# Kernel optimization log

Hardware: AMD Instinct MI355X
Metric: run time of the kernel (lower is better)

Reference implementation:

```python
import jax, jax.numpy as jnp
import numpy as np

NUM_HEADS = 8
HIDDEN = 256


def _coattention(qf, rf, Wq, bq, Wk, bk, Wv, bv, Wo, bo, rel_emb):
    # qf, rf: (b, c, h, w); attention is axial over the height axis per width column.
    b, c, h, w = qf.shape
    T = rel_emb.shape[0]  # 2*max(h,w)-1
    q_in = qf.reshape(b, c, h * w).transpose(0, 2, 1)  # b (hw) c
    r_in = rf.reshape(b, c, h * w).transpose(0, 2, 1)
    q = (q_in @ Wq + bq).reshape(b, h, w, NUM_HEADS, HIDDEN).transpose(0, 3, 1, 2, 4)  # b n h w c
    k = (r_in @ Wk + bk).reshape(b, h, w, NUM_HEADS, HIDDEN).transpose(0, 3, 1, 2, 4)
    v = (r_in @ Wv + bv).reshape(b, h, w, NUM_HEADS, HIDDEN).transpose(0, 3, 1, 2, 4)
    scores = jnp.einsum('bnhwc,bnkwc->bnhwk', q, k)
    # relative index table: idx[i, j] = j - i, wrapped like torch negative indexing
    idx_h = (jnp.arange(h)[None, :] - jnp.arange(h)[:, None]) % T  # (h, h)
    idx_w = (jnp.arange(w)[None, :] - jnp.arange(w)[:, None]) % T  # (w, w); h == w required
    rel_h = rel_emb[idx_h]  # (h, h, c)
    rel_w = rel_emb[idx_w]  # (w, w, c)
    scores = scores + jnp.einsum('bnhwc,hkc->bnhwk', q, rel_h)
    scores = scores + jnp.einsum('bnhwc,wkc->bnhwk', q, rel_w)
    probs = jax.nn.softmax(scores / np.float32(np.sqrt(HIDDEN)), axis=-1)
    att = jnp.einsum('bnhwk,bnkwc->bnhwc', probs, v)
    out = att.transpose(0, 2, 3, 1, 4).reshape(b, h * w, NUM_HEADS * HIDDEN)  # b (hw) (n c)
    out = out @ Wo + bo
    return out.transpose(0, 2, 1).reshape(b, c, h, w)


def setup_inputs() -> dict:
    key = jax.random.key(0)
    ks = jax.random.split(key, 8)
    B, C, H, W = 4, 2048, 32, 32
    s = np.float32(0.02)
    return {
        'left_features': jax.random.normal(ks[0], (B, C, H, W), jnp.float32),
        'right_features': jax.random.normal(ks[1], (B, C, H, W), jnp.float32),
        'Wq': jax.random.normal(ks[2], (C, C), jnp.float32) * s,
        'bq': jnp.zeros((C,), jnp.float32),
        'Wk': jax.random.normal(ks[3], (C, C), jnp.float32) * s,
        'bk': jnp.zeros((C,), jnp.float32),
        'Wv': jax.random.normal(ks[4], (C, C), jnp.float32) * s,
        'bv': jnp.zeros((C,), jnp.float32),
        'Wo': jax.random.normal(ks[5], (C, C), jnp.float32) * s,
        'bo': jnp.zeros((C,), jnp.float32),
        'rel_emb': jax.random.normal(ks[6], (2 * max(H, W) - 1, HIDDEN), jnp.float32),
    }


def reference(left_features, right_features, Wq, bq, Wk, bk, Wv, bv, Wo, bo, rel_emb):
    weighted_r = _coattention(left_features, right_features, Wq, bq, Wk, bk, Wv, bv, Wo, bo, rel_emb)
    weighted_l = _coattention(right_features, left_features, Wq, bq, Wk, bk, Wv, bv, Wo, bo, rel_emb)
    left_attended = jnp.concatenate([left_features, weighted_r], axis=1)
    right_attended = jnp.concatenate([right_features, weighted_l], axis=1)
    return (left_attended, right_attended)
```

## Files before the change

### kernel.cpp

```cpp
#include <hip/hip_runtime.h>
#include <hip/hip_bf16.h>

typedef __attribute__((ext_vector_type(8))) short bf16x8;
typedef __attribute__((ext_vector_type(4))) float f32x4;

#define MFMA16(a, b, c) __builtin_amdgcn_mfma_f32_16x16x32_bf16((a), (b), (c), 0, 0, 0)

typedef __attribute__((address_space(1))) const void gconst_t;
typedef __attribute__((address_space(3))) void lds_t;
__device__ __forceinline__ void gload16(const void* gp, void* lp) {
    __builtin_amdgcn_global_load_lds((gconst_t*)gp, (lds_t*)lp, 16, 0, 0);
}

#define BAR() asm volatile("s_barrier" ::: "memory")
#define VMCNT0() asm volatile("s_waitcnt vmcnt(0)" ::: "memory")
#define DRAIN() asm volatile("s_waitcnt vmcnt(0) lgkmcnt(0)" ::: "memory")
#define PRIO1() __builtin_amdgcn_s_setprio(1)
#define PRIO0() __builtin_amdgcn_s_setprio(0)
#define SCHED0() __builtin_amdgcn_sched_barrier(0)

struct PArgs {
    const float* w[4];
    __hip_bfloat16* wt[4];
    const float* x[2];
    __hip_bfloat16* xb[2];
    const float* rel;
    __hip_bfloat16* relb;
    float* out;
};
__global__ void prep(PArgs pa) {
    __shared__ float tile[32][33];
    const int z = blockIdx.z;
    const int tx = threadIdx.x, ty = threadIdx.y;
    if (z < 4) {
        const float* __restrict__ ib = pa.w[z];
        __hip_bfloat16* __restrict__ ob = pa.wt[z];
        int r0 = blockIdx.y * 32, c0 = blockIdx.x * 32;
#pragma unroll
        for (int i = ty; i < 32; i += 8)
            tile[i][tx] = ib[(size_t)(r0 + i) * 2048 + c0 + tx];
        __syncthreads();
#pragma unroll
        for (int i = ty; i < 32; i += 8)
            ob[(size_t)(c0 + i) * 2048 + r0 + tx] = __float2bfloat16(tile[tx][i]);
    } else {
        const int zb = z - 4;
        const int side = blockIdx.x >> 5;
        size_t zoff = (size_t)zb * 2048 * 1024;
        const float* __restrict__ ib = pa.x[side] + zoff;
        __hip_bfloat16* __restrict__ ob = pa.xb[side] + zoff;
        float* __restrict__ cb = pa.out + (size_t)side * 16777216 + (size_t)zb * 4194304;
        int r0 = blockIdx.y * 32, c0 = (blockIdx.x & 31) * 32;
#pragma unroll
        for (int i = ty; i < 32; i += 8) {
            float v = ib[(size_t)(r0 + i) * 1024 + c0 + tx];
            tile[i][tx] = v;
            cb[(size_t)(r0 + i) * 1024 + c0 + tx] = v;
        }
        __syncthreads();
#pragma unroll
        for (int i = ty; i < 32; i += 8)
            ob[(size_t)(c0 + i) * 2048 + r0 + tx] = __float2bfloat16(tile[tx][i]);
        if (z == 4 && blockIdx.x == 0 && blockIdx.y == 0) {
            int tid = ty * 32 + tx;
            for (int i = tid; i < 64 * 256; i += 256) {
                int r = i >> 8;
                pa.relb[i] = __float2bfloat16(r < 63 ? pa.rel[i] : 0.f);
            }
        }
    }
}

struct GArgs {
    const __hip_bfloat16* A[6];
    const __hip_bfloat16* B[6];
    void* C[6];
    const float* bias[6];
};

template <int MODE>
__global__ __launch_bounds__(512, 2) void gemm8p(GArgs ga, float* __restrict__ dout) {
    constexpr int K = 2048;
    constexpr int NOUT = 2048;
    constexpr int NT = 32;
    __shared__ __align__(16) char smem[131072];

    const int gx = gridDim.x, gy = gridDim.y;
    int lid = blockIdx.x + gx * (blockIdx.y + gy * blockIdx.z);
    const int nwg = gx * gy * gridDim.z;
    int swz = (lid & 7) * (nwg >> 3) + (lid >> 3);
    const int z = swz / (gx * gy);
    int rem = swz - z * (gx * gy);
    const int by = rem / gx;
    const int bx = rem - by * gx;

    const __hip_bfloat16* __restrict__ A = ga.A[z];
    const __hip_bfloat16* __restrict__ B = ga.B[z];
    const float* __restrict__ bias = ga.bias[z];
    const int row0 = by * 256, col0 = bx * 256;

    const int tid = threadIdx.x;
    const int wave = tid >> 6, lane = tid & 63;
    const int l15 = lane & 15, lg = lane >> 4;
    const int wm = wave >> 2, wn = wave & 3;

    const int srow = tid >> 3;
    const int sch = (tid & 7) ^ (srow & 7);
    const int xr = (l15 & 7) << 4;
    const int off0 = (lg * 16) ^ xr;
    const int off1 = (64 + lg * 16) ^ xr;

    f32x4 acc[8][4] = {};
    bf16x8 aL[4][2], aH[4][2], bL[2][2], bH[2][2];

    auto ST = [&](const __hip_bfloat16* base, int rowb, int T, int buf, int isB, int h) {
#pragma unroll
        for (int L = 0; L < 2; ++L)
            gload16(base + (size_t)(rowb + h * 128 + L * 64 + srow) * K + T * 64 + sch * 8,
                    smem + buf * 65536 + isB * 32768 + h * 16384 + L * 8192 + tid * 16);
    };

#define RD_A(DST, C, MH)                                                           \
    _Pragma("unroll") for (int mf = 0; mf < 4; ++mf) {                             \
        const char* p = smem + (C) * 65536 + (wm * 128 + (MH) * 64 + mf * 16 + l15) * 128; \
        DST[mf][0] = *(const bf16x8*)(p + off0);                                   \
        DST[mf][1] = *(const bf16x8*)(p + off1);                                   \
    }
#define RD_B(DST, C, NH)                                                           \
    _Pragma("unroll") for (int nf = 0; nf < 2; ++nf) {                             \
        const char* p = smem + (C) * 65536 + 32768 +                               \
                        (wn * 64 + (NH) * 32 + nf * 16 + l15) * 128;               \
        DST[nf][0] = *(const bf16x8*)(p + off0);                                   \
        DST[nf][1] = *(const bf16x8*)(p + off1);                                   \
    }
#define MQ(MH, NH, AR, BR)                                                         \
    SCHED0();                                                                      \
    PRIO1();                                                                       \
    _Pragma("unroll") for (int mf = 0; mf < 4; ++mf)                               \
    _Pragma("unroll") for (int nf = 0; nf < 2; ++nf) {                             \
        acc[(MH)*4 + mf][(NH)*2 + nf] =                                            \
            MFMA16(AR[mf][0], BR[nf][0], acc[(MH)*4 + mf][(NH)*2 + nf]);           \
        acc[(MH)*4 + mf][(NH)*2 + nf] =                                            \
            MFMA16(AR[mf][1], BR[nf][1], acc[(MH)*4 + mf][(NH)*2 + nf]);           \
    }                                                                              \
    PRIO0();

#define KTILE(T, C)                                          \
    {                                                        \
        const int tn = ((T) + 1 < NT) ? (T) + 1 : (T)-1;     \
                                                     \
        RD_A(aL, C, 0);                                      \
        RD_B(bL, C, 0);                                      \
        ST(A, row0, tn, (C) ^ 1, 0, 0);                      \
        ST(B, col0, tn, (C) ^ 1, 1, 0);                      \
        BAR();                                               \
        MQ(0, 0, aL, bL);                                    \
                                                     \
        RD_B(bH, C, 1);                                      \
        ST(A, row0, tn, (C) ^ 1, 0, 1);                      \
        ST(B, col0, tn, (C) ^ 1, 1, 1);                      \
        BAR();                                               \
        MQ(0, 1, aL, bH);                                    \
                                                     \
        RD_A(aH, C, 1);                                      \
        BAR();                                               \
        MQ(1, 1, aH, bH);                                    \
                                                     \
        VMCNT0();                                            \
        BAR();                                               \
        MQ(1, 0, aH, bL);                                    \
    }

    ST(A, row0, 0, 0, 0, 0);
    ST(A, row0, 0, 0, 0, 1);
    ST(B, col0, 0, 0, 1, 0);
    ST(B, col0, 0, 0, 1, 1);
    VMCNT0();
    BAR();

#pragma unroll 1
    for (int t = 0; t < NT; t += 2) {
        KTILE(t, 0);
        KTILE(t + 1, 1);
    }
    DRAIN();

    if (MODE == 0) {
        __hip_bfloat16* __restrict__ C = (__hip_bfloat16*)ga.C[z];
#pragma unroll
        for (int mf = 0; mf < 8; ++mf) {
            int m = row0 + wm * 128 + mf * 16 + lg * 4;
#pragma unroll
            for (int nf = 0; nf < 4; ++nf) {
                int n = col0 + wn * 64 + nf * 16 + l15;
                float bv = bias[n];
#pragma unroll
                for (int r = 0; r < 4; ++r)
                    C[(size_t)(m + r) * NOUT + n] = __float2bfloat16(acc[mf][nf][r] + bv);
            }
        }
    } else {
        float* __restrict__ OB = dout + (size_t)z * 16777216;
#pragma unroll
        for (int mf = 0; mf < 8; ++mf) {
            int n0 = row0 + wm * 128 + mf * 16 + lg * 4;
#pragma unroll
            for (int nf = 0; nf < 4; ++nf) {
                int m = col0 + wn * 64 + nf * 16 + l15;
                size_t base = (size_t)(m >> 10) * 4194304 + (size_t)(m & 1023);
#pragma unroll
                for (int r = 0; r < 4; ++r) {
                    int n = n0 + r;
                    OB[base + (size_t)(2048 + n) * 1024] = acc[mf][nf][r] + bias[n];
                }
            }
        }
    }
#undef RD_A
#undef RD_B
#undef MQ
#undef KTILE
}

__global__ __launch_bounds__(256, 2) void attn_kernel(
    const __hip_bfloat16* __restrict__ Qa, const __hip_bfloat16* __restrict__ Ka,
    const __hip_bfloat16* __restrict__ Va, const __hip_bfloat16* __restrict__ Qb,
    const __hip_bfloat16* __restrict__ Kb, const __hip_bfloat16* __restrict__ Vb,
    const __hip_bfloat16* __restrict__ relb, __hip_bfloat16* __restrict__ Oa,
    __hip_bfloat16* __restrict__ Ob) {
    const int w = blockIdx.x;
    const int nh = blockIdx.y;
    const int zb = blockIdx.z;
    const int dir = zb >> 2, b = zb & 3;
    const __hip_bfloat16* __restrict__ Q = dir ? Qb : Qa;
    const __hip_bfloat16* __restrict__ K = dir ? Kb : Ka;
    const __hip_bfloat16* __restrict__ V = dir ? Vb : Va;
    __hip_bfloat16* __restrict__ O = dir ? Ob : Oa;

    __shared__ __align__(16) __hip_bfloat16 vt[256 * 40];
    __shared__ float ssc[32 * 32];
    __shared__ float es[32 * 64];
    __shared__ __align__(16) __hip_bfloat16 ps[32 * 32];

    const int tid = threadIdx.x;
    const int lane = tid & 63, wave = tid >> 6;
    const int l15 = lane & 15, lg = lane >> 4;
    const int mt = wave >> 1, nt = wave & 1;

    const size_t rowbase = ((size_t)b * 1024 + w) * 2048 + (size_t)nh * 256;

    for (int i = 0; i < 32; ++i) {
        int e = i * 256 + tid;
        int hk = e >> 8, c = e & 255;
        vt[c * 40 + hk] = V[rowbase + (size_t)hk * 65536 + c];
    }

    f32x4 sacc = {}, e0 = {}, e1 = {};
#pragma unroll
    for (int k8 = 0; k8 < 256; k8 += 32) {
        bf16x8 af = *(const bf16x8*)&Q[rowbase + (size_t)(mt * 16 + l15) * 65536 + k8 + lg * 8];
        bf16x8 bf = *(const bf16x8*)&K[rowbase + (size_t)(nt * 16 + l15) * 65536 + k8 + lg * 8];
        bf16x8 r0 = *(const bf16x8*)&relb[(size_t)(nt * 32 + l15) * 256 + k8 + lg * 8];
        bf16x8 r1 = *(const bf16x8*)&relb[(size_t)(nt * 32 + 16 + l15) * 256 + k8 + lg * 8];
        sacc = MFMA16(af, bf, sacc);
        e0 = MFMA16(af, r0, e0);
        e1 = MFMA16(af, r1, e1);
    }
#pragma unroll
    for (int r = 0; r < 4; ++r) {
        int row = mt * 16 + lg * 4 + r;
        ssc[row * 32 + nt * 16 + l15] = sacc[r];
        es[row * 64 + nt * 32 + l15] = e0[r];
        es[row * 64 + nt * 32 + 16 + l15] = e1[r];
    }
    __syncthreads();

    {
        int h = tid >> 3, sub = tid & 7;
        float v4[4];
        float mx = -1e30f;
#pragma unroll
        for (int i = 0; i < 4; ++i) {
            int k = sub * 4 + i;
            int dh = k - h; if (dh < 0) dh += 63;
            int dw = k - w; if (dw < 0) dw += 63;
            float s = (ssc[h * 32 + k] + es[h * 64 + dh] + es[h * 64 + dw]) * 0.0625f;
            v4[i] = s;
            mx = fmaxf(mx, s);
        }
        mx = fmaxf(mx, __shfl_xor(mx, 1));
        mx = fmaxf(mx, __shfl_xor(mx, 2));
        mx = fmaxf(mx, __shfl_xor(mx, 4));
        float sum = 0.f;
#pragma unroll
        for (int i = 0; i < 4; ++i) {
            v4[i] = __expf(v4[i] - mx);
            sum += v4[i];
        }
        sum += __shfl_xor(sum, 1);
        sum += __shfl_xor(sum, 2);
        sum += __shfl_xor(sum, 4);
        float inv = 1.f / sum;
#pragma unroll
        for (int i = 0; i < 4; ++i) ps[h * 32 + sub * 4 + i] = __float2bfloat16(v4[i] * inv);
    }
    __syncthreads();

    bf16x8 paf = *(const bf16x8*)&ps[(mt * 16 + l15) * 32 + lg * 8];
#pragma unroll
    for (int j = 0; j < 8; ++j) {
        int ct = nt * 8 + j;
        bf16x8 bv = *(const bf16x8*)&vt[(size_t)(ct * 16 + l15) * 40 + lg * 8];
        f32x4 oacc = {};
        oacc = MFMA16(paf, bv, oacc);
#pragma unroll
        for (int r = 0; r < 4; ++r) {
            int hh = mt * 16 + lg * 4 + r;
            O[rowbase + (size_t)hh * 65536 + ct * 16 + l15] = __float2bfloat16(oacc[r]);
        }
    }
}

extern "C" void kernel_launch(void* const* d_in, const int* in_sizes, int n_in, void* d_out,
                              int out_size, void* d_ws, size_t ws_size, hipStream_t stream) {
    const float* Xl = (const float*)d_in[0];
    const float* Xr = (const float*)d_in[1];
    const float* Wq = (const float*)d_in[2];
    const float* bq = (const float*)d_in[3];
    const float* Wk = (const float*)d_in[4];
    const float* bk = (const float*)d_in[5];
    const float* Wv = (const float*)d_in[6];
    const float* bv = (const float*)d_in[7];
    const float* Wo = (const float*)d_in[8];
    const float* bo = (const float*)d_in[9];
    const float* rel = (const float*)d_in[10];
    float* out = (float*)d_out;

    char* ws = (char*)d_ws;
    size_t off = 0;
    auto nxt = [&](size_t bytes) {
        void* p = ws + off;
        off += bytes;
        return p;
    };
    __hip_bfloat16* Xbl = (__hip_bfloat16*)nxt(16777216);
    __hip_bfloat16* Xbr = (__hip_bfloat16*)nxt(16777216);
    __hip_bfloat16* Wtq = (__hip_bfloat16*)nxt(8388608);
    __hip_bfloat16* Wtk = (__hip_bfloat16*)nxt(8388608);
    __hip_bfloat16* Wtv = (__hip_bfloat16*)nxt(8388608);
    __hip_bfloat16* Wto = (__hip_bfloat16*)nxt(8388608);
    __hip_bfloat16* relb = (__hip_bfloat16*)nxt(32768);
    __hip_bfloat16* Ql = (__hip_bfloat16*)nxt(16777216);
    __hip_bfloat16* Kl = (__hip_bfloat16*)nxt(16777216);
    __hip_bfloat16* Vl = (__hip_bfloat16*)nxt(16777216);
    __hip_bfloat16* Qr = (__hip_bfloat16*)nxt(16777216);
    __hip_bfloat16* Kr = (__hip_bfloat16*)nxt(16777216);
    __hip_bfloat16* Vr = (__hip_bfloat16*)nxt(16777216);
    __hip_bfloat16* At0 = Xbl;
    __hip_bfloat16* At1 = Xbr;

    PArgs pa;
    pa.w[0] = Wq; pa.w[1] = Wk; pa.w[2] = Wv; pa.w[3] = Wo;
    pa.wt[0] = Wtq; pa.wt[1] = Wtk; pa.wt[2] = Wtv; pa.wt[3] = Wto;
    pa.x[0] = Xl; pa.x[1] = Xr;
    pa.xb[0] = Xbl; pa.xb[1] = Xbr;
    pa.rel = rel; pa.relb = relb; pa.out = out;
    prep<<<dim3(64, 64, 8), dim3(32, 8), 0, stream>>>(pa);

    GArgs g1 = {};
    g1.A[0] = Xbl; g1.A[1] = Xbl; g1.A[2] = Xbl;
    g1.A[3] = Xbr; g1.A[4] = Xbr; g1.A[5] = Xbr;
    g1.B[0] = Wtq; g1.B[1] = Wtk; g1.B[2] = Wtv;
    g1.B[3] = Wtq; g1.B[4] = Wtk; g1.B[5] = Wtv;
    g1.C[0] = Ql; g1.C[1] = Kl; g1.C[2] = Vl;
    g1.C[3] = Qr; g1.C[4] = Kr; g1.C[5] = Vr;
    g1.bias[0] = bq; g1.bias[1] = bk; g1.bias[2] = bv;
    g1.bias[3] = bq; g1.bias[4] = bk; g1.bias[5] = bv;
    gemm8p<0><<<dim3(8, 16, 6), 512, 0, stream>>>(g1, nullptr);

    attn_kernel<<<dim3(32, 8, 8), 256, 0, stream>>>(Ql, Kr, Vr, Qr, Kl, Vl, relb, At0, At1);

    GArgs g2 = {};
    g2.A[0] = Wto; g2.A[1] = Wto;
    g2.B[0] = At0; g2.B[1] = At1;
    g2.bias[0] = bo; g2.bias[1] = bo;
    gemm8p<1><<<dim3(16, 8, 2), 512, 0, stream>>>(g2, out);
}
```

Before: 347.7 us.

## Deepen GEMM load pipeline by prefetching quarter-tiles two K-steps ahead

Splits global-to-LDS staging into 64-row quarters and issues each quarter as soon as the LDS region it overwrites has been consumed. Parts of tile T+2 are written into the current buffer while tile T is still being computed, with the rest of T+1 going into the other buffer. The full vmcnt(0) wait becomes vmcnt(6), so loads stay in flight across the tile boundary. This hides more global load latency, but the correctness of the buffer reuse depends on tight ordering of barriers and wait counts.

```diff
diff --git a/kernel.cpp b/kernel.cpp
--- a/kernel.cpp
+++ b/kernel.cpp
@@ -14,6 +14,7 @@
 
 #define BAR() asm volatile("s_barrier" ::: "memory")
 #define VMCNT0() asm volatile("s_waitcnt vmcnt(0)" ::: "memory")
+#define VMCNT6() asm volatile("s_waitcnt vmcnt(6)" ::: "memory")
 #define DRAIN() asm volatile("s_waitcnt vmcnt(0) lgkmcnt(0)" ::: "memory")
 #define PRIO1() __builtin_amdgcn_s_setprio(1)
 #define PRIO0() __builtin_amdgcn_s_setprio(0)
@@ -113,11 +114,9 @@
     f32x4 acc[8][4] = {};
     bf16x8 aL[4][2], aH[4][2], bL[2][2], bH[2][2];
 
-    auto ST = [&](const __hip_bfloat16* base, int rowb, int T, int buf, int isB, int h) {
-#pragma unroll
-        for (int L = 0; L < 2; ++L)
-            gload16(base + (size_t)(rowb + h * 128 + L * 64 + srow) * K + T * 64 + sch * 8,
-                    smem + buf * 65536 + isB * 32768 + h * 16384 + L * 8192 + tid * 16);
+    auto STQ = [&](const __hip_bfloat16* base, int rowb, int T, int buf, int isB, int q) {
+        gload16(base + (size_t)(rowb + q * 64 + srow) * K + T * 64 + sch * 8,
+                smem + buf * 65536 + isB * 32768 + q * 8192 + tid * 16);
     };
 
 #define RD_A(DST, C, MH)                                                           \
@@ -147,35 +146,47 @@
 
 #define KTILE(T, C)                                          \
     {                                                        \
-        const int tn = ((T) + 1 < NT) ? (T) + 1 : (T)-1;     \
+        const int tn1 = ((T) + 1 < NT) ? (T) + 1 : (T)-1;    \
+        const int tn2 = ((T) + 2 < NT) ? (T) + 2 : (T);      \
                                                      \
         RD_A(aL, C, 0);                                      \
         RD_B(bL, C, 0);                                      \
-        ST(A, row0, tn, (C) ^ 1, 0, 0);                      \
-        ST(B, col0, tn, (C) ^ 1, 1, 0);                      \
+        STQ(A, row0, tn1, (C) ^ 1, 0, 1);                    \
+        STQ(A, row0, tn1, (C) ^ 1, 0, 3);                    \
         BAR();                                               \
         MQ(0, 0, aL, bL);                                    \
                                                      \
         RD_B(bH, C, 1);                                      \
-        ST(A, row0, tn, (C) ^ 1, 0, 1);                      \
-        ST(B, col0, tn, (C) ^ 1, 1, 1);                      \
+        STQ(A, row0, tn2, (C), 0, 0);                        \
+        STQ(A, row0, tn2, (C), 0, 2);                        \
         BAR();                                               \
         MQ(0, 1, aL, bH);                                    \
                                                      \
         RD_A(aH, C, 1);                                      \
+        STQ(B, col0, tn2, (C), 1, 0);                        \
+        STQ(B, col0, tn2, (C), 1, 1);                        \
         BAR();                                               \
         MQ(1, 1, aH, bH);                                    \
                                                      \
-        VMCNT0();                                            \
+        STQ(B, col0, tn2, (C), 1, 2);                        \
+        STQ(B, col0, tn2, (C), 1, 3);                        \
+        VMCNT6();                                            \
         BAR();                                               \
         MQ(1, 0, aH, bL);                                    \
     }
 
-    ST(A, row0, 0, 0, 0, 0);
-    ST(A, row0, 0, 0, 0, 1);
-    ST(B, col0, 0, 0, 1, 0);
-    ST(B, col0, 0, 0, 1, 1);
-    VMCNT0();
+#pragma unroll
+    for (int q = 0; q < 4; ++q) {
+        STQ(A, row0, 0, 0, 0, q);
+        STQ(B, col0, 0, 0, 1, q);
+    }
+    STQ(A, row0, 1, 1, 0, 0);
+    STQ(A, row0, 1, 1, 0, 2);
+    STQ(B, col0, 1, 1, 1, 0);
+    STQ(B, col0, 1, 1, 1, 1);
+    STQ(B, col0, 1, 1, 1, 2);
+    STQ(B, col0, 1, 1, 1, 3);
+    VMCNT6();
     BAR();
 
 #pragma unroll 1
```

New measurement: 344.2 us. No clear change (-1.0%).
